# Kernel optimization log

Hardware: AMD Instinct MI355X
Metric: run time of the kernel (lower is better)

Reference implementation:

```python
import jax, jax.numpy as jnp
import numpy as np

GAMMA = 1.0  # get_gamma(1, None) == 1


def setup_inputs() -> dict:
    key = jax.random.key(0)
    # scale down so recursion divisors 1 - km^2 stay well-conditioned
    a = jax.random.normal(key, (2048, 1024, 33), dtype=jnp.float32) * 0.05
    return {"a": a}


def reference(a):
    # LPC -> PARCOR (reverse Levinson-Durbin recursion), a: [..., M+1]
    M = a.shape[-1] - 1
    K = a[..., :1]          # gain term, passed through
    ar = a[..., 1:] * GAMMA  # working LPC coefficients, length M
    ks = []
    # Python loop over the (small, fixed) LPC order; fully vectorized over batch.
    for m in range(M - 1, -1, -1):
        km = ar[..., m:m + 1]           # reflection coefficient k_m
        ks.append(km)
        if m == 0:
            break
        z = 1.0 - km * km
        k = ar[..., :m]                 # step-down: shrink order by one
        ar = (k - km * k[..., ::-1]) / z
    ks.append(K)
    return jnp.concatenate(ks[::-1], axis=-1)
```

## Files before the change

kernel.cpp:

```cpp
#include <hip/hip_runtime.h>

#define M 32
#define NC 33
#define TPB 128
#define FPB (TPB * NC)
#define V4 8
#define TAIL (V4 * 4 * TPB)

typedef float f4 __attribute__((ext_vector_type(4)));

__device__ __forceinline__ void levinson(float* __restrict__ lds, int rb) {
    float ar[M];
#pragma unroll
    for (int j = 0; j < M; ++j) ar[j] = lds[rb + 1 + j];
#pragma unroll
    for (int m = M - 1; m >= 1; --m) {
        float km = ar[m];
        lds[rb + m + 1] = km;
        float z = 1.0f - km * km;
        float r = 1.0f / z;
        const int h = m >> 1;
#pragma unroll
        for (int j = 0; j < h; ++j) {
            float x = ar[j], y = ar[m - 1 - j];
            ar[j]         = (x - km * y) * r;
            ar[m - 1 - j] = (y - km * x) * r;
        }
        if (m & 1) ar[h] = (ar[h] - km * ar[h]) * r;
    }
    lds[rb + 1] = ar[0];
}

__device__ __forceinline__ void load_tile_full(float* __restrict__ lds,
                                               const float* __restrict__ src, int t) {
    const f4* a4 = (const f4*)src;
    f4* l4 = (f4*)lds;
#pragma unroll
    for (int k = 0; k < V4; ++k) l4[t + k * TPB] = a4[t + k * TPB];
    lds[TAIL + t] = src[TAIL + t];
}

__device__ __forceinline__ void store_tile_nt(float* __restrict__ dst,
                                              const float* __restrict__ lds, int t) {
    const f4* l4 = (const f4*)lds;
#pragma unroll
    for (int k = 0; k < V4; ++k) {
        f4 v = l4[t + k * TPB];
        __builtin_nontemporal_store(v, (f4*)dst + t + k * TPB);
    }
    __builtin_nontemporal_store(lds[TAIL + t], dst + TAIL + t);
}

__device__ __forceinline__ void process_tile_guarded(float* __restrict__ lds,
                                                     const float* __restrict__ a,
                                                     float* __restrict__ out,
                                                     long long base, long long limit, int t) {
    for (int k = 0; k < NC; ++k) {
        int g = t + k * TPB;
        long long ga = base + g;
        lds[g] = (ga < limit) ? a[ga] : 0.0f;
    }
    __syncthreads();
    levinson(lds, t * NC);
    __syncthreads();
    for (int k = 0; k < NC; ++k) {
        int g = t + k * TPB;
        long long ga = base + g;
        if (ga < limit) out[ga] = lds[g];
    }
    __syncthreads();
}

__global__ __launch_bounds__(TPB)
void lpc_to_parcor_kernel(const float* __restrict__ a,
                          float* __restrict__ out,
                          long long nrows) {
    __shared__ float lds[FPB];
    const int t = threadIdx.x;
    const long long limit = nrows * NC;
    const long long base0 = (long long)blockIdx.x * 2 * FPB;
    const long long base1 = base0 + FPB;
    const bool full0 = (base0 + FPB) <= limit;
    const bool full1 = (base1 + FPB) <= limit;

    if (full0 && full1) {
        load_tile_full(lds, a + base0, t);
        __syncthreads();

        f4 p[V4]; float pt;
        {
            const f4* b4 = (const f4*)(a + base1);
#pragma unroll
            for (int k = 0; k < V4; ++k) p[k] = b4[t + k * TPB];
            pt = a[base1 + TAIL + t];
        }
        __builtin_amdgcn_sched_barrier(0);

        levinson(lds, t * NC);
        __syncthreads();

        store_tile_nt(out + base0, lds, t);
        __syncthreads();

        {
            f4* l4 = (f4*)lds;
#pragma unroll
            for (int k = 0; k < V4; ++k) l4[t + k * TPB] = p[k];
            lds[TAIL + t] = pt;
        }
        __syncthreads();

        levinson(lds, t * NC);
        __syncthreads();

        store_tile_nt(out + base1, lds, t);
    } else {
        if (base0 < limit) process_tile_guarded(lds, a, out, base0, limit, t);
        if (base1 < limit) process_tile_guarded(lds, a, out, base1, limit, t);
    }
}

extern "C" void kernel_launch(void* const* d_in, const int* in_sizes, int n_in,
                              void* d_out, int out_size, void* d_ws, size_t ws_size,
                              hipStream_t stream) {
    const float* a = (const float*)d_in[0];
    float* out = (float*)d_out;
    long long nrows = (long long)in_sizes[0] / NC;
    long long tiles = (nrows + TPB - 1) / TPB;
    long long blocks = (tiles + 1) / 2;
    lpc_to_parcor_kernel<<<(int)blocks, TPB, 0, stream>>>(a, out, nrows);
}
```

Before: 94.80 us.

## Make blocks loop over multiple tiles with register prefetch of next tile

Launches a capped grid of 2048 blocks, each looping over a contiguous range of tiles. While one tile is processed, the next tile's input is prefetched into registers. The aim is to overlap global loads with Levinson compute across a longer per-block pipeline and to cut block scheduling overhead. The trade-off is fewer resident blocks overall, which may reduce memory-level parallelism and latency hiding.

```diff
diff --git a/kernel.cpp b/kernel.cpp
--- a/kernel.cpp
+++ b/kernel.cpp
@@ -6,6 +6,7 @@
 #define FPB (TPB * NC)
 #define V4 8
 #define TAIL (V4 * 4 * TPB)
+#define NBLOCKS 2048
 
 typedef float f4 __attribute__((ext_vector_type(4)));
 
@@ -29,15 +30,6 @@
         if (m & 1) ar[h] = (ar[h] - km * ar[h]) * r;
     }
     lds[rb + 1] = ar[0];
-}
-
-__device__ __forceinline__ void load_tile_full(float* __restrict__ lds,
-                                               const float* __restrict__ src, int t) {
-    const f4* a4 = (const f4*)src;
-    f4* l4 = (f4*)lds;
-#pragma unroll
-    for (int k = 0; k < V4; ++k) l4[t + k * TPB] = a4[t + k * TPB];
-    lds[TAIL + t] = src[TAIL + t];
 }
 
 __device__ __forceinline__ void store_tile_nt(float* __restrict__ dst,
@@ -74,49 +66,54 @@
 __global__ __launch_bounds__(TPB)
 void lpc_to_parcor_kernel(const float* __restrict__ a,
                           float* __restrict__ out,
-                          long long nrows) {
+                          long long nrows, long long tiles_per_block) {
     __shared__ float lds[FPB];
     const int t = threadIdx.x;
     const long long limit = nrows * NC;
-    const long long base0 = (long long)blockIdx.x * 2 * FPB;
-    const long long base1 = base0 + FPB;
-    const bool full0 = (base0 + FPB) <= limit;
-    const bool full1 = (base1 + FPB) <= limit;
+    const long long ntiles = (nrows + TPB - 1) / TPB;
+    const long long nfull  = nrows / TPB;
 
-    if (full0 && full1) {
-        load_tile_full(lds, a + base0, t);
-        __syncthreads();
+    long long t0 = (long long)blockIdx.x * tiles_per_block;
+    long long t1 = t0 + tiles_per_block; if (t1 > ntiles) t1 = ntiles;
+    if (t0 >= t1) return;
+    long long fend = (t1 < nfull) ? t1 : nfull;
 
+    if (t0 < fend) {
         f4 p[V4]; float pt;
         {
-            const f4* b4 = (const f4*)(a + base1);
+            const float* src = a + t0 * FPB;
+            const f4* s4 = (const f4*)src;
 #pragma unroll
-            for (int k = 0; k < V4; ++k) p[k] = b4[t + k * TPB];
-            pt = a[base1 + TAIL + t];
+            for (int k = 0; k < V4; ++k) p[k] = s4[t + k * TPB];
+            pt = src[TAIL + t];
         }
-        __builtin_amdgcn_sched_barrier(0);
+        for (long long ti = t0; ti < fend; ++ti) {
+            {
+                f4* l4 = (f4*)lds;
+#pragma unroll
+                for (int k = 0; k < V4; ++k) l4[t + k * TPB] = p[k];
+                lds[TAIL + t] = pt;
+            }
+            __syncthreads();
 
-        levinson(lds, t * NC);
+            if (ti + 1 < fend) {
+                const float* src = a + (ti + 1) * FPB;
+                const f4* s4 = (const f4*)src;
+#pragma unroll
+                for (int k = 0; k < V4; ++k) p[k] = s4[t + k * TPB];
+                pt = src[TAIL + t];
+            }
+            __builtin_amdgcn_sched_barrier(0);
+
+            levinson(lds, t * NC);
+            __syncthreads();
+
+            store_tile_nt(out + ti * FPB, lds, t);
+        }
+    }
+    for (long long ti = (t0 > nfull ? t0 : nfull); ti < t1; ++ti) {
         __syncthreads();
-
-        store_tile_nt(out + base0, lds, t);
-        __syncthreads();
-
-        {
-            f4* l4 = (f4*)lds;
-#pragma unroll
-            for (int k = 0; k < V4; ++k) l4[t + k * TPB] = p[k];
-            lds[TAIL + t] = pt;
-        }
-        __syncthreads();
-
-        levinson(lds, t * NC);
-        __syncthreads();
-
-        store_tile_nt(out + base1, lds, t);
-    } else {
-        if (base0 < limit) process_tile_guarded(lds, a, out, base0, limit, t);
-        if (base1 < limit) process_tile_guarded(lds, a, out, base1, limit, t);
+        process_tile_guarded(lds, a, out, ti * FPB, limit, t);
     }
 }
 
@@ -126,7 +123,8 @@
     const float* a = (const float*)d_in[0];
     float* out = (float*)d_out;
     long long nrows = (long long)in_sizes[0] / NC;
-    long long tiles = (nrows + TPB - 1) / TPB;
-    long long blocks = (tiles + 1) / 2;
-    lpc_to_parcor_kernel<<<(int)blocks, TPB, 0, stream>>>(a, out, nrows);
+    long long ntiles = (nrows + TPB - 1) / TPB;
+    long long blocks = (ntiles < NBLOCKS) ? ntiles : NBLOCKS;
+    long long tpb_tiles = (ntiles + blocks - 1) / blocks;
+    lpc_to_parcor_kernel<<<(int)blocks, TPB, 0, stream>>>(a, out, nrows, tpb_tiles);
 }
```

After: 102.9 us. 1.09x slower.
